# Optimization experiments

Hardware: AMD Instinct MI355X
Metric: run time of the kernel (lower is better)

Reference implementation:

```python
import jax, jax.numpy as jnp
import numpy as np

D_MODEL = 64  # per-head dim; temper = sqrt(D_MODEL)
NEG_INF = -1e30  # stand-in for -inf; safe under softmax and autodiff


def setup_inputs() -> dict:
    key = jax.random.key(0)
    kq, kk, kv, km = jax.random.split(key, 4)
    B, S, D = 16, 2048, 64
    q = jax.random.normal(kq, (B, S, D), dtype=jnp.float32)
    k = jax.random.normal(kk, (B, S, D), dtype=jnp.float32)
    v = jax.random.normal(kv, (B, S, D), dtype=jnp.float32)
    attn_mask = jax.random.bernoulli(km, 0.1, (B, S, S))
    return {"q": q, "k": k, "v": v, "attn_mask": attn_mask}


def reference(q, k, v, attn_mask):
    temper = jnp.sqrt(jnp.float32(D_MODEL))
    # [B, Sq, Sk] scores
    attn = jnp.einsum("bqd,bkd->bqk", q, k) / temper
    attn = jnp.where(attn_mask, NEG_INF, attn)
    attn = jax.nn.softmax(attn, axis=2)
    # dropout is identity in eval / attn_dropout=0.0
    output = jnp.einsum("bqk,bkd->bqd", attn, v)
    return (output, attn)
```

## Files before the change

### kernel.cpp

```cpp
#include <hip/hip_runtime.h>
#include <hip/hip_bf16.h>
#include <stdint.h>


#define S_DIM 2048
#define D_DIM 64

typedef short short8 __attribute__((ext_vector_type(8)));
typedef float floatx4 __attribute__((ext_vector_type(4)));
typedef unsigned short ushort8v __attribute__((ext_vector_type(8)));
typedef uint32_t u32a __attribute__((may_alias));

__device__ __forceinline__ unsigned short f2bf(float x) {
    uint32_t u = __float_as_uint(x);
    u += 0x7fffu + ((u >> 16) & 1u);
    return (unsigned short)(u >> 16);
}
__device__ __forceinline__ float bf2f(unsigned short h) {
    return __uint_as_float((uint32_t)h << 16);
}

__global__ __launch_bounds__(256) void prep_all(
    const int* __restrict__ mask, uint32_t* __restrict__ bits,
    const float* __restrict__ k,
    unsigned short* __restrict__ khi2, unsigned short* __restrict__ klo2,
    const float* __restrict__ v, unsigned short* __restrict__ vfrag)
{
    const int blk = blockIdx.x;
    const int tid = threadIdx.x;

    if (blk < 8192) {
        const size_t base = (size_t)blk * 8192;
        const int lane = tid & 63;
        const size_t wbase = base + (size_t)(tid & ~63);
        #pragma unroll
        for (int j = 0; j < 32; ++j) {
            int m = mask[base + j * 256 + tid];
            unsigned long long bal = __ballot(m != 0);
            if ((lane & 31) == 0) {
                size_t wb = wbase + j * 256;
                bits[(wb >> 5) + (lane >> 5)] = (uint32_t)(bal >> ((lane >> 5) * 32));
            }
        }
    } else if (blk < 9216) {
        const int e  = blk - 8192;
        const int b  = e >> 6;
        const int kc = (e & 63) * 2 + (tid >> 7);
        const int t  = tid & 127;
        const int s = t >> 6, quad = (t >> 4) & 3, n16 = t & 15;
        const float* src = k + ((size_t)(b * S_DIM) + kc * 16 + n16) * D_DIM + s * 32 + quad * 8;
        float4 x0 = *(const float4*)src;
        float4 x1 = *(const float4*)(src + 4);
        float xs[8] = {x0.x, x0.y, x0.z, x0.w, x1.x, x1.y, x1.z, x1.w};
        ushort8v h, l;
        #pragma unroll
        for (int p = 0; p < 8; ++p) {
            unsigned short hp = f2bf(xs[p]);
            h[p] = hp;
            l[p] = f2bf(xs[p] - bf2f(hp));
        }
        size_t o = ((size_t)(b * 128 + kc)) * 1024 + (size_t)t * 8;
        *(ushort8v*)(khi2 + o) = h;
        *(ushort8v*)(klo2 + o) = l;
    } else {
        const int e  = blk - 9216;
        const int b  = e >> 6;
        const int kb = e & 63;
        const int nc = tid >> 6, quad = (tid >> 4) & 3, n16 = tid & 15;
        ushort8v o;
        #pragma unroll
        for (int p = 0; p < 8; ++p) {
            float x = v[((size_t)(b * S_DIM) + kb * 32 + quad * 8 + p) * D_DIM + nc * 16 + n16];
            o[p] = f2bf(x);
        }
        *(ushort8v*)(vfrag + ((size_t)(b * 64 + kb)) * 2048 + (size_t)tid * 8) = o;
    }
}

__global__ __launch_bounds__(1024) void attn_fused_v6(
    const float* __restrict__ q,
    const unsigned short* __restrict__ khi2, const unsigned short* __restrict__ klo2,
    const unsigned short* __restrict__ vfrag,
    const uint32_t* __restrict__ bits,
    float* __restrict__ out, float* __restrict__ attn)
{
    __shared__ __align__(16) float qlds[16 * 68];
    __shared__ __align__(16) unsigned short pbuf[16 * 16 * 36];
    __shared__ __align__(16) float obuf[8 * 16 * 68];
    __shared__ float mxtab[16 * 16];
    __shared__ float ltab[16 * 16];

    const int tid  = threadIdx.x;
    const int w    = tid >> 6;
    const int lane = tid & 63;
    const int quad = lane >> 4;
    const int n16  = lane & 15;
    const int wg   = blockIdx.x;
    const int swz  = (wg & 7) * 256 + (wg >> 3);
    const int b    = swz >> 7;
    const int q0   = (swz & 127) * 16;
    const int key0 = w * 128;

    uint32_t bmask = bits[((size_t)(b * S_DIM) + q0 + (lane >> 2)) * 64 + w * 4 + (lane & 3)];

    {
        int m = tid >> 6, d = tid & 63;
        qlds[m * 68 + d] = q[((size_t)(b * S_DIM + q0 + m)) * D_DIM + d];
    }
    __syncthreads();

    short8 ahi[2], alo[2];
    #pragma unroll
    for (int s = 0; s < 2; ++s) {
        const float* qp = &qlds[n16 * 68 + s * 32 + quad * 8];
        union { unsigned short u[8]; short8 v; } H, L;
        #pragma unroll
        for (int p = 0; p < 8; ++p) {
            float x = qp[p];
            unsigned short hp = f2bf(x);
            H.u[p] = hp;
            L.u[p] = f2bf(x - bf2f(hp));
        }
        ahi[s] = H.v; alo[s] = L.v;
    }

    floatx4 sc[8];
    const unsigned short* khb = khi2 + (size_t)b * 131072;
    const unsigned short* klb = klo2 + (size_t)b * 131072;
    #pragma unroll
    for (int c = 0; c < 8; ++c) {
        const int kc = w * 8 + c;
        floatx4 acc = {0.f, 0.f, 0.f, 0.f};
        #pragma unroll
        for (int s = 0; s < 2; ++s) {
            const size_t off = (size_t)((kc * 2 + s) * 4 + quad) * 128 + n16 * 8;
            short8 BH = *(const short8*)(khb + off);
            short8 BL = *(const short8*)(klb + off);
            acc = __builtin_amdgcn_mfma_f32_16x16x32_bf16(ahi[s], BH, acc, 0, 0, 0);
            acc = __builtin_amdgcn_mfma_f32_16x16x32_bf16(ahi[s], BL, acc, 0, 0, 0);
            acc = __builtin_amdgcn_mfma_f32_16x16x32_bf16(alo[s], BH, acc, 0, 0, 0);
        }
        sc[c] = acc;
    }
    #pragma unroll
    for (int r = 0; r < 4; ++r) {
        #pragma unroll
        for (int c = 0; c < 8; ++c) {
            int srcl = (quad * 4 + r) * 4 + (c >> 1);
            uint32_t d = (uint32_t)__shfl((int)bmask, srcl, 64);
            uint32_t bit = (d >> ((c & 1) * 16 + n16)) & 1u;
            sc[c][r] = bit ? -1e30f : sc[c][r] * 0.125f;
        }
    }

    #pragma unroll
    for (int r = 0; r < 4; ++r) {
        float mx = sc[0][r];
        #pragma unroll
        for (int c = 1; c < 8; ++c) mx = fmaxf(mx, sc[c][r]);
        #pragma unroll
        for (int o = 1; o < 16; o <<= 1) mx = fmaxf(mx, __shfl_xor(mx, o, 64));
        if (n16 == 0) mxtab[w * 16 + quad * 4 + r] = mx;
    }
    __syncthreads();
    #pragma unroll
    for (int r = 0; r < 4; ++r) {
        float mf = -3e38f;
        #pragma unroll
        for (int w2 = 0; w2 < 16; ++w2) mf = fmaxf(mf, mxtab[w2 * 16 + quad * 4 + r]);
        float l = 0.f;
        #pragma unroll
        for (int c = 0; c < 8; ++c) {
            float e = __expf(sc[c][r] - mf);
            sc[c][r] = e;
            l += e;
        }
        #pragma unroll
        for (int o = 1; o < 16; o <<= 1) l += __shfl_xor(l, o, 64);
        if (n16 == 0) ltab[w * 16 + quad * 4 + r] = l;
    }
    __syncthreads();
    #pragma unroll
    for (int r = 0; r < 4; ++r) {
        float l = 0.f;
        #pragma unroll
        for (int w2 = 0; w2 < 16; ++w2) l += ltab[w2 * 16 + quad * 4 + r];
        float inv = 1.0f / l;
        #pragma unroll
        for (int c = 0; c < 8; ++c) sc[c][r] *= inv;
    }

    {
        float* arow = attn + (size_t)(b * S_DIM + q0 + quad * 4) * S_DIM + key0 + n16;
        #pragma unroll
        for (int c = 0; c < 8; ++c) {
            #pragma unroll
            for (int r = 0; r < 4; ++r) arow[(size_t)r * S_DIM + c * 16] = sc[c][r];
        }
    }

    floatx4 o0 = {0,0,0,0}, o1 = {0,0,0,0}, o2 = {0,0,0,0}, o3 = {0,0,0,0};
    unsigned short* pw = pbuf + w * 576;
    const unsigned short* vtb = vfrag + (size_t)b * 131072;
    #pragma unroll
    for (int s2 = 0; s2 < 4; ++s2) {
        #pragma unroll
        for (int h = 0; h < 2; ++h) {
            const int c = s2 * 2 + h;
            #pragma unroll
            for (int r = 0; r < 4; ++r)
                pw[(quad * 4 + r) * 36 + h * 16 + n16] = f2bf(sc[c][r]);
        }
        short8 pa;
        {
            const u32a* pr = (const u32a*)((const char*)pbuf +
                                   (size_t)w * 1152 + n16 * 72 + quad * 16);
            union { uint32_t u[4]; short8 v; } P;
            P.u[0] = pr[0]; P.u[1] = pr[1]; P.u[2] = pr[2]; P.u[3] = pr[3];
            pa = P.v;
        }
        const int kb = w * 4 + s2;
        #pragma unroll
        for (int nc = 0; nc < 4; ++nc) {
            const size_t off = (size_t)((kb * 4 + nc) * 4 + quad) * 128 + n16 * 8;
            short8 bv = *(const short8*)(vtb + off);
            floatx4& oo = (nc == 0 ? o0 : nc == 1 ? o1 : nc == 2 ? o2 : o3);
            oo = __builtin_amdgcn_mfma_f32_16x16x32_bf16(pa, bv, oo, 0, 0, 0);
        }
    }

    if (w < 8) {
        #pragma unroll
        for (int nc = 0; nc < 4; ++nc) {
            floatx4 oo = (nc == 0 ? o0 : nc == 1 ? o1 : nc == 2 ? o2 : o3);
            #pragma unroll
            for (int i = 0; i < 4; ++i)
                obuf[(w * 16 + quad * 4 + i) * 68 + nc * 16 + n16] = oo[i];
        }
    }
    __syncthreads();
    if (w >= 8) {
        #pragma unroll
        for (int nc = 0; nc < 4; ++nc) {
            floatx4 oo = (nc == 0 ? o0 : nc == 1 ? o1 : nc == 2 ? o2 : o3);
            #pragma unroll
            for (int i = 0; i < 4; ++i)
                obuf[((w - 8) * 16 + quad * 4 + i) * 68 + nc * 16 + n16] += oo[i];
        }
    }
    __syncthreads();
    {
        int m = tid >> 6, d = tid & 63;
        float a = 0.f;
        #pragma unroll
        for (int w2 = 0; w2 < 8; ++w2) a += obuf[(w2 * 16 + m) * 68 + d];
        out[(size_t)(b * S_DIM + q0 + m) * D_DIM + d] = a;
    }
}

__global__ __launch_bounds__(512) void attn_fused_v1(
    const float* __restrict__ q, const float* __restrict__ k,
    const float* __restrict__ v, const int* __restrict__ mask,
    float* __restrict__ out, float* __restrict__ attn)
{
    __shared__ __align__(16) float qlds[16 * 68];
    __shared__ __align__(16) unsigned short pbuf[8 * 16 * 36];
    __shared__ __align__(16) float obuf[8 * 16 * 68];
    __shared__ float mxtab[8 * 16];
    __shared__ float ltab[8 * 16];

    const int tid  = threadIdx.x;
    const int w    = tid >> 6;
    const int lane = tid & 63;
    const int quad = lane >> 4;
    const int n16  = lane & 15;
    const int b    = blockIdx.x >> 7;
    const int q0   = (blockIdx.x & 127) * 16;
    const int key0 = w * 256;

    {
        int m = tid >> 5, d = (tid & 31) * 2;
        float2 qv = *(const float2*)(q + ((size_t)(b * S_DIM + q0 + m)) * D_DIM + d);
        qlds[m * 68 + d]     = qv.x;
        qlds[m * 68 + d + 1] = qv.y;
    }
    __syncthreads();

    short8 ahi[2], alo[2];
    #pragma unroll
    for (int s = 0; s < 2; ++s) {
        const float* qp = &qlds[n16 * 68 + s * 32 + quad * 8];
        union { __hip_bfloat162 h[4]; short8 v; } H, L;
        #pragma unroll
        for (int p = 0; p < 4; ++p) {
            float x0 = qp[2 * p], x1 = qp[2 * p + 1];
            __hip_bfloat162 h2 = __float22bfloat162_rn(float2{x0, x1});
            float l0 = x0 - __bfloat162float(h2.x);
            float l1 = x1 - __bfloat162float(h2.y);
            H.h[p] = h2;
            L.h[p] = __float22bfloat162_rn(float2{l0, l1});
        }
        ahi[s] = H.v; alo[s] = L.v;
    }

    floatx4 sc[16];
    const size_t kvbase = (size_t)(b * S_DIM) * D_DIM;
    #pragma unroll
    for (int c = 0; c < 16; ++c) {
        const int key = key0 + c * 16 + n16;
        const int* mp = mask + (size_t)(b * S_DIM + q0 + quad * 4) * S_DIM + key;
        int mk0 = mp[0], mk1 = mp[S_DIM], mk2 = mp[2 * S_DIM], mk3 = mp[3 * S_DIM];
        floatx4 acc = {0.f, 0.f, 0.f, 0.f};
        #pragma unroll
        for (int s = 0; s < 2; ++s) {
            const float* kp = k + kvbase + (size_t)key * D_DIM + s * 32 + quad * 8;
            float4 k0 = *(const float4*)kp;
            float4 k1 = *(const float4*)(kp + 4);
            float kf[8] = {k0.x, k0.y, k0.z, k0.w, k1.x, k1.y, k1.z, k1.w};
            union { __hip_bfloat162 h[4]; short8 v; } BH, BL;
            #pragma unroll
            for (int p = 0; p < 4; ++p) {
                float x0 = kf[2 * p], x1 = kf[2 * p + 1];
                __hip_bfloat162 h2 = __float22bfloat162_rn(float2{x0, x1});
                BH.h[p] = h2;
                BL.h[p] = __float22bfloat162_rn(
                    float2{x0 - __bfloat162float(h2.x), x1 - __bfloat162float(h2.y)});
            }
            acc = __builtin_amdgcn_mfma_f32_16x16x32_bf16(ahi[s], BH.v, acc, 0, 0, 0);
            acc = __builtin_amdgcn_mfma_f32_16x16x32_bf16(ahi[s], BL.v, acc, 0, 0, 0);
            acc = __builtin_amdgcn_mfma_f32_16x16x32_bf16(alo[s], BH.v, acc, 0, 0, 0);
        }
        sc[c][0] = mk0 ? -1e30f : acc[0] * 0.125f;
        sc[c][1] = mk1 ? -1e30f : acc[1] * 0.125f;
        sc[c][2] = mk2 ? -1e30f : acc[2] * 0.125f;
        sc[c][3] = mk3 ? -1e30f : acc[3] * 0.125f;
    }

    #pragma unroll
    for (int r = 0; r < 4; ++r) {
        float mx = sc[0][r];
        #pragma unroll
        for (int c = 1; c < 16; ++c) mx = fmaxf(mx, sc[c][r]);
        #pragma unroll
        for (int o = 1; o < 16; o <<= 1) mx = fmaxf(mx, __shfl_xor(mx, o, 64));
        if (n16 == 0) mxtab[w * 16 + quad * 4 + r] = mx;
    }
    __syncthreads();
    #pragma unroll
    for (int r = 0; r < 4; ++r) {
        float mf = -3e38f;
        #pragma unroll
        for (int w2 = 0; w2 < 8; ++w2) mf = fmaxf(mf, mxtab[w2 * 16 + quad * 4 + r]);
        float l = 0.f;
        #pragma unroll
        for (int c = 0; c < 16; ++c) {
            float e = __expf(sc[c][r] - mf);
            sc[c][r] = e;
            l += e;
        }
        #pragma unroll
        for (int o = 1; o < 16; o <<= 1) l += __shfl_xor(l, o, 64);
        if (n16 == 0) ltab[w * 16 + quad * 4 + r] = l;
    }
    __syncthreads();
    #pragma unroll
    for (int r = 0; r < 4; ++r) {
        float l = 0.f;
        #pragma unroll
        for (int w2 = 0; w2 < 8; ++w2) l += ltab[w2 * 16 + quad * 4 + r];
        float inv = 1.0f / l;
        #pragma unroll
        for (int c = 0; c < 16; ++c) sc[c][r] *= inv;
    }

    {
        float* arow = attn + (size_t)(b * S_DIM + q0 + quad * 4) * S_DIM + key0 + n16;
        #pragma unroll
        for (int c = 0; c < 16; ++c) {
            #pragma unroll
            for (int r = 0; r < 4; ++r) arow[(size_t)r * S_DIM + c * 16] = sc[c][r];
        }
    }

    floatx4 o0 = {0,0,0,0}, o1 = {0,0,0,0}, o2 = {0,0,0,0}, o3 = {0,0,0,0};
    unsigned short* pw = pbuf + w * 576;
    #pragma unroll
    for (int s2 = 0; s2 < 8; ++s2) {
        #pragma unroll
        for (int h = 0; h < 2; ++h) {
            const int c = s2 * 2 + h;
            #pragma unroll
            for (int r = 0; r < 4; ++r)
                pw[(quad * 4 + r) * 36 + h * 16 + n16] = f2bf(sc[c][r]);
        }
        __syncthreads();
        short8 pa;
        {
            const uint32_t* pr = (const uint32_t*)((const char*)pbuf +
                                   (size_t)w * 1152 + n16 * 72 + quad * 16);
            union { uint32_t u[4]; short8 v; } P;
            P.u[0] = pr[0]; P.u[1] = pr[1]; P.u[2] = pr[2]; P.u[3] = pr[3];
            pa = P.v;
        }
        const size_t vrow0 = (size_t)(b * S_DIM + key0 + s2 * 32 + quad * 8) * D_DIM;
        #pragma unroll
        for (int nc = 0; nc < 4; ++nc) {
            const float* vp = v + vrow0 + nc * 16 + n16;
            union { __hip_bfloat162 h[4]; short8 v8; } BV;
            #pragma unroll
            for (int p = 0; p < 4; ++p) {
                float x0 = vp[(size_t)(2 * p) * D_DIM];
                float x1 = vp[(size_t)(2 * p + 1) * D_DIM];
                BV.h[p] = __float22bfloat162_rn(float2{x0, x1});
            }
            floatx4& oo = (nc == 0 ? o0 : nc == 1 ? o1 : nc == 2 ? o2 : o3);
            oo = __builtin_amdgcn_mfma_f32_16x16x32_bf16(pa, BV.v8, oo, 0, 0, 0);
        }
        __syncthreads();
    }

    #pragma unroll
    for (int nc = 0; nc < 4; ++nc) {
        floatx4 oo = (nc == 0 ? o0 : nc == 1 ? o1 : nc == 2 ? o2 : o3);
        #pragma unroll
        for (int i = 0; i < 4; ++i)
            obuf[(w * 16 + quad * 4 + i) * 68 + nc * 16 + n16] = oo[i];
    }
    __syncthreads();
    #pragma unroll
    for (int t2 = 0; t2 < 2; ++t2) {
        int idx = tid + t2 * 512;
        int m = idx >> 6, d = idx & 63;
        float a = 0.f;
        #pragma unroll
        for (int w2 = 0; w2 < 8; ++w2) a += obuf[(w2 * 16 + m) * 68 + d];
        out[(size_t)(b * S_DIM + q0 + m) * D_DIM + d] = a;
    }
}

extern "C" void kernel_launch(void* const* d_in, const int* in_sizes, int n_in,
                              void* d_out, int out_size, void* d_ws, size_t ws_size,
                              hipStream_t stream) {
    const float* q    = (const float*)d_in[0];
    const float* k    = (const float*)d_in[1];
    const float* v    = (const float*)d_in[2];
    const int*   mask = (const int*)d_in[3];

    float* out  = (float*)d_out;
    float* attn = out + (size_t)16 * S_DIM * D_DIM;

    const size_t NE = (size_t)16 * S_DIM * D_DIM;
    const size_t need = NE * 2 * 3 + NE * 4;
    if (d_ws != nullptr && ws_size >= need) {
        unsigned short* khi2  = (unsigned short*)d_ws;
        unsigned short* klo2  = khi2 + NE;
        unsigned short* vfrag = klo2 + NE;
        uint32_t*       bits  = (uint32_t*)(vfrag + NE);
        prep_all<<<dim3(10240), dim3(256), 0, stream>>>(mask, bits, k, khi2, klo2, v, vfrag);
        attn_fused_v6<<<dim3(2048), dim3(1024), 0, stream>>>(q, khi2, klo2, vfrag, bits, out, attn);
    } else {
        attn_fused_v1<<<dim3(2048), dim3(512), 0, stream>>>(q, k, v, mask, out, attn);
    }
}
```

Before: 557.7 us.

## Fuse mask bit-packing into attention kernel, read int mask directly

Removes the separate mask-to-bitmask pass from the prep kernel. The attention kernel now loads the raw int mask rows itself with int4 loads and packs them into per-lane bit words via ballots. This avoids writing and re-reading the packed bits buffer and a large serial prep phase, so the mask read can overlap with attention compute. In exchange, each block issues more global loads and ballot work, and register pressure rises.

```diff
diff --git a/kernel.cpp b/kernel.cpp
--- a/kernel.cpp
+++ b/kernel.cpp
@@ -20,8 +20,7 @@
     return __uint_as_float((uint32_t)h << 16);
 }
 
-__global__ __launch_bounds__(256) void prep_all(
-    const int* __restrict__ mask, uint32_t* __restrict__ bits,
+__global__ __launch_bounds__(256) void prep_kv(
     const float* __restrict__ k,
     unsigned short* __restrict__ khi2, unsigned short* __restrict__ klo2,
     const float* __restrict__ v, unsigned short* __restrict__ vfrag)
@@ -29,21 +28,8 @@
     const int blk = blockIdx.x;
     const int tid = threadIdx.x;
 
-    if (blk < 8192) {
-        const size_t base = (size_t)blk * 8192;
-        const int lane = tid & 63;
-        const size_t wbase = base + (size_t)(tid & ~63);
-        #pragma unroll
-        for (int j = 0; j < 32; ++j) {
-            int m = mask[base + j * 256 + tid];
-            unsigned long long bal = __ballot(m != 0);
-            if ((lane & 31) == 0) {
-                size_t wb = wbase + j * 256;
-                bits[(wb >> 5) + (lane >> 5)] = (uint32_t)(bal >> ((lane >> 5) * 32));
-            }
-        }
-    } else if (blk < 9216) {
-        const int e  = blk - 8192;
+    if (blk < 1024) {
+        const int e  = blk;
         const int b  = e >> 6;
         const int kc = (e & 63) * 2 + (tid >> 7);
         const int t  = tid & 127;
@@ -63,7 +49,7 @@
         *(ushort8v*)(khi2 + o) = h;
         *(ushort8v*)(klo2 + o) = l;
     } else {
-        const int e  = blk - 9216;
+        const int e  = blk - 1024;
         const int b  = e >> 6;
         const int kb = e & 63;
         const int nc = tid >> 6, quad = (tid >> 4) & 3, n16 = tid & 15;
@@ -77,11 +63,11 @@
     }
 }
 
-__global__ __launch_bounds__(1024) void attn_fused_v6(
+__global__ __launch_bounds__(1024) void attn_fused_v7(
     const float* __restrict__ q,
     const unsigned short* __restrict__ khi2, const unsigned short* __restrict__ klo2,
     const unsigned short* __restrict__ vfrag,
-    const uint32_t* __restrict__ bits,
+    const int* __restrict__ mask,
     float* __restrict__ out, float* __restrict__ attn)
 {
     __shared__ __align__(16) float qlds[16 * 68];
@@ -101,7 +87,14 @@
     const int q0   = (swz & 127) * 16;
     const int key0 = w * 128;
 
-    uint32_t bmask = bits[((size_t)(b * S_DIM) + q0 + (lane >> 2)) * 64 + w * 4 + (lane & 3)];
+    int4 mx[8];
+    {
+        const int* mrow = mask + ((size_t)(b * S_DIM) + q0 + (lane >> 5)) * S_DIM
+                               + key0 + (lane & 31) * 4;
+        #pragma unroll
+        for (int it = 0; it < 8; ++it)
+            mx[it] = *(const int4*)(mrow + (size_t)(2 * it) * S_DIM);
+    }
 
     {
         int m = tid >> 6, d = tid & 63;
@@ -122,6 +115,23 @@
             L.u[p] = f2bf(x - bf2f(hp));
         }
         ahi[s] = H.v; alo[s] = L.v;
+    }
+
+    uint32_t kept = 0;
+    {
+        const int lr = lane >> 2;
+        const int le = lane & 3;
+        #pragma unroll
+        for (int it = 0; it < 8; ++it) {
+            #pragma unroll
+            for (int e = 0; e < 4; ++e) {
+                int val = (e == 0 ? mx[it].x : e == 1 ? mx[it].y
+                         : e == 2 ? mx[it].z : mx[it].w);
+                unsigned long long bal = __ballot(val != 0);
+                if (lr == 2 * it && le == e)     kept = (uint32_t)bal;
+                if (lr == 2 * it + 1 && le == e) kept = (uint32_t)(bal >> 32);
+            }
+        }
     }
 
     floatx4 sc[8];
@@ -144,23 +154,23 @@
     }
     #pragma unroll
     for (int r = 0; r < 4; ++r) {
+        int srcl = (quad * 4 + r) * 4 + (n16 & 3);
+        uint32_t wd = (uint32_t)__shfl((int)kept, srcl, 64);
         #pragma unroll
         for (int c = 0; c < 8; ++c) {
-            int srcl = (quad * 4 + r) * 4 + (c >> 1);
-            uint32_t d = (uint32_t)__shfl((int)bmask, srcl, 64);
-            uint32_t bit = (d >> ((c & 1) * 16 + n16)) & 1u;
+            uint32_t bit = (wd >> (c * 4 + (n16 >> 2))) & 1u;
             sc[c][r] = bit ? -1e30f : sc[c][r] * 0.125f;
         }
     }
 
     #pragma unroll
     for (int r = 0; r < 4; ++r) {
-        float mx = sc[0][r];
-        #pragma unroll
-        for (int c = 1; c < 8; ++c) mx = fmaxf(mx, sc[c][r]);
-        #pragma unroll
-        for (int o = 1; o < 16; o <<= 1) mx = fmaxf(mx, __shfl_xor(mx, o, 64));
-        if (n16 == 0) mxtab[w * 16 + quad * 4 + r] = mx;
+        float mxv = sc[0][r];
+        #pragma unroll
+        for (int c = 1; c < 8; ++c) mxv = fmaxf(mxv, sc[c][r]);
+        #pragma unroll
+        for (int o = 1; o < 16; o <<= 1) mxv = fmaxf(mxv, __shfl_xor(mxv, o, 64));
+        if (n16 == 0) mxtab[w * 16 + quad * 4 + r] = mxv;
     }
     __syncthreads();
     #pragma unroll
@@ -450,14 +460,13 @@
     float* attn = out + (size_t)16 * S_DIM * D_DIM;
 
     const size_t NE = (size_t)16 * S_DIM * D_DIM;
-    const size_t need = NE * 2 * 3 + NE * 4;
+    const size_t need = NE * 2 * 3;
     if (d_ws != nullptr && ws_size >= need) {
         unsigned short* khi2  = (unsigned short*)d_ws;
         unsigned short* klo2  = khi2 + NE;
         unsigned short* vfrag = klo2 + NE;
-        uint32_t*       bits  = (uint32_t*)(vfrag + NE);
-        prep_all<<<dim3(10240), dim3(256), 0, stream>>>(mask, bits, k, khi2, klo2, v, vfrag);
-        attn_fused_v6<<<dim3(2048), dim3(1024), 0, stream>>>(q, khi2, klo2, vfrag, bits, out, attn);
+        prep_kv<<<dim3(2048), dim3(256), 0, stream>>>(k, khi2, klo2, v, vfrag);
+        attn_fused_v7<<<dim3(2048), dim3(1024), 0, stream>>>(q, khi2, klo2, vfrag, mask, out, attn);
     } else {
         attn_fused_v1<<<dim3(2048), dim3(512), 0, stream>>>(q, k, v, mask, out, attn);
     }
```

New measurement: 556.0 us. No clear change (-0.3%).
